# Kernel optimization log

Measured on AMD Instinct MI355X. Metric: run time of the kernel, lower is better.

Reference implementation:

```python
import jax, jax.numpy as jnp
from jax import lax
import numpy as np

B, C, H, W = 4, 64, 64, 64
D_STATE, D_CONV = 16, 4


def setup_inputs() -> dict:
    key = jax.random.key(0)
    ks = iter(jax.random.split(key, 64))
    def rnd(shape, s=0.02):
        return jax.random.normal(next(ks), shape, jnp.float32) * s
    inp = {}
    inp["x"] = jax.random.normal(next(ks), (B, C, H, W), jnp.float32)
    # LayerNorm((C,H,W)) affine params
    inp["n1_w"] = jnp.ones((C, H, W), jnp.float32); inp["n1_b"] = jnp.zeros((C, H, W), jnp.float32)
    inp["n2_w"] = jnp.ones((C, H, W), jnp.float32); inp["n2_b"] = jnp.zeros((C, H, W), jnp.float32)
    # OSSModule projections
    inp["inproj_w"] = rnd((2 * C, C)); inp["inproj_b"] = jnp.zeros((2 * C,), jnp.float32)
    inp["dw_w"] = rnd((C, 1, 3, 3), 0.1); inp["dw_b"] = jnp.zeros((C,), jnp.float32)
    inp["outproj_w"] = rnd((C, C)); inp["outproj_b"] = jnp.zeros((C,), jnp.float32)
    # Mamba params (expand=2, d_state=16, d_conv=4, dt_rank=ceil(d_model/16))
    def mamba_p(name, d_model):
        d_inner = 2 * d_model
        dt_rank = max(1, -(-d_model // 16))
        inp[name + "_in_w"] = rnd((2 * d_inner, d_model))
        inp[name + "_conv_w"] = rnd((d_inner, 1, D_CONV), 0.1)
        inp[name + "_conv_b"] = jnp.zeros((d_inner,), jnp.float32)
        inp[name + "_xproj_w"] = rnd((dt_rank + 2 * D_STATE, d_inner))
        inp[name + "_dt_w"] = rnd((d_inner, dt_rank), dt_rank ** -0.5)
        inp[name + "_dt_b"] = jnp.full((d_inner,), -4.6, jnp.float32)  # softplus -> ~0.01
        inp[name + "_Alog"] = jnp.log(jnp.tile(jnp.arange(1, D_STATE + 1, dtype=jnp.float32), (d_inner, 1)))
        inp[name + "_D"] = jnp.ones((d_inner,), jnp.float32)
        inp[name + "_out_w"] = rnd((d_model, d_inner))
    mamba_p("m1", 4 * C)
    mamba_p("m2", 2)
    # EFFN (hidden = 2*C)
    hid = 2 * C
    inp["ffn_in_w"] = rnd((2 * hid, C)); inp["ffn_in_b"] = jnp.zeros((2 * hid,), jnp.float32)
    inp["ffn_dw_w"] = rnd((2 * hid, 1, 3, 3), 0.1); inp["ffn_dw_b"] = jnp.zeros((2 * hid,), jnp.float32)
    inp["ffn_out_w"] = rnd((C, hid)); inp["ffn_out_b"] = jnp.zeros((C,), jnp.float32)
    return inp


def layernorm(x, w, b, eps=1e-5):
    mu = x.mean((1, 2, 3), keepdims=True)
    var = ((x - mu) ** 2).mean((1, 2, 3), keepdims=True)
    return (x - mu) * lax.rsqrt(var + eps) * w + b


def conv1x1(x, w, b):
    return jnp.einsum('oi,bihw->bohw', w, x) + b[None, :, None, None]


def dwconv3(x, w, b):
    y = lax.conv_general_dilated(x, w, (1, 1), [(1, 1), (1, 1)],
                                 dimension_numbers=('NCHW', 'OIHW', 'NCHW'),
                                 feature_group_count=x.shape[1])
    return y + b[None, :, None, None]


def mamba(u, in_w, conv_w, conv_b, xproj_w, dt_w, dt_b, Alog, Dp, out_w):
    # u: (B, L, d_model) -> (B, L, d_model); faithful mamba_ssm Mamba forward
    Bt, L, _ = u.shape
    d_inner = Alog.shape[0]
    dt_rank = dt_w.shape[1]
    xz = u @ in_w.T
    xi, z = jnp.split(xz, 2, axis=-1)
    # causal depthwise conv over the sequence axis
    xc = lax.conv_general_dilated(xi.transpose(0, 2, 1), conv_w, (1,), [(D_CONV - 1, 0)],
                                  dimension_numbers=('NCH', 'OIH', 'NCH'),
                                  feature_group_count=d_inner)
    xi = jax.nn.silu(xc.transpose(0, 2, 1) + conv_b)
    x_dbl = xi @ xproj_w.T
    dt = jax.nn.softplus(x_dbl[..., :dt_rank] @ dt_w.T + dt_b)      # (B,L,d_inner)
    Bm = x_dbl[..., dt_rank:dt_rank + D_STATE]                      # (B,L,d_state)
    Cm = x_dbl[..., dt_rank + D_STATE:]                             # (B,L,d_state)
    A = -jnp.exp(Alog)                                              # (d_inner,d_state)
    dA = jnp.exp(dt[..., None] * A)                                 # (B,L,d_inner,d_state)
    dBu = (dt * xi)[..., None] * Bm[:, :, None, :]                  # (B,L,d_inner,d_state)
    def step(hst, t):
        dA_t, dBu_t, C_t = t
        hst = dA_t * hst + dBu_t
        return hst, jnp.einsum('bds,bs->bd', hst, C_t)
    h0 = jnp.zeros((Bt, d_inner, D_STATE), u.dtype)
    _, ys = lax.scan(step, h0, (dA.transpose(1, 0, 2, 3), dBu.transpose(1, 0, 2, 3), Cm.transpose(1, 0, 2)))
    y = ys.transpose(1, 0, 2) + xi * Dp
    y = y * jax.nn.silu(z)
    return y @ out_w.T


def reference(x, n1_w, n1_b, n2_w, n2_b, inproj_w, inproj_b, dw_w, dw_b, outproj_w, outproj_b,
              m1_in_w, m1_conv_w, m1_conv_b, m1_xproj_w, m1_dt_w, m1_dt_b, m1_Alog, m1_D, m1_out_w,
              m2_in_w, m2_conv_w, m2_conv_b, m2_xproj_w, m2_dt_w, m2_dt_b, m2_Alog, m2_D, m2_out_w,
              ffn_in_w, ffn_in_b, ffn_dw_w, ffn_dw_b, ffn_out_w, ffn_out_b):
    b, c2, h, w = x.shape
    c = c2
    # --- OSS module branch (pre-norm) ---
    xn = layernorm(x, n1_w, n1_b)
    fo = conv1x1(xn, inproj_w, inproj_b)
    fo1, fo2 = jnp.split(fo, 2, axis=1)
    fo1 = jax.nn.silu(dwconv3(fo1, dw_w, dw_b))
    fo2 = jax.nn.silu(fo2)
    # omni selective scan: 4 directional flattenings concatenated on channels
    hf = fo1.transpose(0, 2, 3, 1).reshape(b, h * w, c)   # row-major (h_forward)
    wf = fo1.transpose(0, 3, 2, 1).reshape(b, h * w, c)   # col-major (w_forward)
    fop = jnp.concatenate([hf, hf[:, ::-1], wf, wf[:, ::-1]], axis=2)  # (b, hw, 4c)
    fop = mamba(fop, m1_in_w, m1_conv_w, m1_conv_b, m1_xproj_w, m1_dt_w, m1_dt_b, m1_Alog, m1_D, m1_out_w)
    fop = fop.reshape(b, h * w, 4, c).sum(2)
    fop = fop.transpose(0, 2, 1).reshape(b, c, h, w)
    residual = fop * fo2
    foc = residual.mean((2, 3))[:, :, None]               # adaptive_avg_pool2d -> (b,c,1)
    foc = jnp.concatenate([foc, foc[:, ::-1]], axis=2)    # (b, c, 2)
    foc = mamba(foc, m2_in_w, m2_conv_w, m2_conv_b, m2_xproj_w, m2_dt_w, m2_dt_b, m2_Alog, m2_D, m2_out_w)
    foc = foc.sum(2)[:, :, None, None]
    foss = foc * residual + residual
    x = conv1x1(foss, outproj_w, outproj_b) + x
    # --- EFFN branch (pre-norm) ---
    g = layernorm(x, n2_w, n2_b)
    g = conv1x1(g, ffn_in_w, ffn_in_b)
    g = dwconv3(g, ffn_dw_w, ffn_dw_b)
    g1, g2 = jnp.split(g, 2, axis=1)
    g = jax.nn.gelu(g1, approximate=False) * g2
    g = conv1x1(g, ffn_out_w, ffn_out_b)
    return g + x
```

## Files before the change

### kernel.cpp

```cpp
#include <hip/hip_runtime.h>
#include <math.h>


#define DEV static __device__ __forceinline__

DEV float silu_f(float x){ return x / (1.f + __expf(-x)); }

DEV ushort f2bf(float f){
  uint u = __float_as_uint(f);
  uint r = (u + 0x7FFF + ((u>>16)&1)) >> 16;
  return (ushort)r;
}
DEV uint f2bf2(float lo, float hi){
  return (uint)f2bf(lo) | ((uint)f2bf(hi)<<16);
}
DEV float bf2f(ushort u){ return __uint_as_float(((uint)u)<<16); }
DEV float bflo(uint u){ return __uint_as_float(u<<16); }
DEV float bfhi(uint u){ return __uint_as_float(u&0xffff0000u); }

typedef __attribute__((ext_vector_type(8))) short bf8_t;
typedef __attribute__((ext_vector_type(4))) float f4_t;

DEV float quad_sum4(float v){
  v += __int_as_float(__builtin_amdgcn_update_dpp(0, __float_as_int(v), 0xB1, 0xF, 0xF, false));
  v += __int_as_float(__builtin_amdgcn_update_dpp(0, __float_as_int(v), 0x4E, 0xF, 0xF, false));
  return v;
}
template<int O> DEV uint qb(uint v){
  return (uint)__builtin_amdgcn_update_dpp(0, (int)v, O*0x55, 0xF, 0xF, false);
}

__global__ __launch_bounds__(256) void ln_part(const float* __restrict__ x,
                                               float2* __restrict__ part){
  int blk = blockIdx.x; int b = blk>>6, pc = blk&63;
  const float* p = x + (size_t)b*262144 + (size_t)pc*4096;
  float s=0.f, s2=0.f;
  #pragma unroll
  for(int it=0; it<4; ++it){
    int i = threadIdx.x + it*256;
    float4 v = *(const float4*)(p + i*4);
    s  += v.x+v.y+v.z+v.w;
    s2 += v.x*v.x+v.y*v.y+v.z*v.z+v.w*v.w;
  }
  __shared__ float ls[256], ls2[256];
  ls[threadIdx.x]=s; ls2[threadIdx.x]=s2; __syncthreads();
  for(int st=128;st>0;st>>=1){
    if(threadIdx.x<st){ ls[threadIdx.x]+=ls[threadIdx.x+st]; ls2[threadIdx.x]+=ls2[threadIdx.x+st]; }
    __syncthreads();
  }
  if(threadIdx.x==0) part[blk]=make_float2(ls[0],ls2[0]);
}
__global__ __launch_bounds__(64) void ln_fin(const float2* __restrict__ part,
                                             float* __restrict__ mu, float* __restrict__ rstd){
  int b = blockIdx.x;
  float2 v = part[b*64+threadIdx.x];
  __shared__ double ds_[64], ds2_[64];
  ds_[threadIdx.x]=v.x; ds2_[threadIdx.x]=v.y; __syncthreads();
  for(int st=32;st>0;st>>=1){
    if(threadIdx.x<st){ ds_[threadIdx.x]+=ds_[threadIdx.x+st]; ds2_[threadIdx.x]+=ds2_[threadIdx.x+st]; }
    __syncthreads();
  }
  if(threadIdx.x==0){
    double m = ds_[0]*(1.0/262144.0);
    double var = ds2_[0]*(1.0/262144.0) - m*m;
    mu[b]=(float)m; rstd[b]=(float)(1.0/sqrt(var+1e-5));
  }
}

__global__ __launch_bounds__(256) void ln1_inproj(const float* __restrict__ x,
    const float* __restrict__ n1w, const float* __restrict__ n1b,
    const float* __restrict__ ipw, const float* __restrict__ ipb,
    const float* __restrict__ mu, const float* __restrict__ rstd,
    float* __restrict__ fo1_raw, float* __restrict__ fo2s){
  int bh = blockIdx.x; int b = bh>>6, h = bh&63;
  __shared__ float xn[64][64];
  __shared__ float wl[128*64];
  float m = mu[b], rs = rstd[b];
  for(int i=threadIdx.x;i<4096;i+=256){
    int c=i>>6, w=i&63;
    size_t sp=(size_t)c*4096 + h*64 + w;
    float v = x[(size_t)b*262144 + sp];
    xn[c][w] = (v-m)*rs*n1w[sp] + n1b[sp];
  }
  for(int i=threadIdx.x;i<8192;i+=256) wl[i]=ipw[i];
  __syncthreads();
  int px = threadIdx.x & 63, ob = (threadIdx.x>>6)*32;
  float acc[32];
  #pragma unroll
  for(int j=0;j<32;j++) acc[j]=0.f;
  for(int c=0;c<64;c++){
    float xv = xn[c][px];
    #pragma unroll
    for(int j=0;j<32;j++) acc[j] = fmaf(wl[(ob+j)*64+c], xv, acc[j]);
  }
  for(int j=0;j<32;j++){
    int o = ob+j;
    float v = acc[j] + ipb[o];
    if(o<64) fo1_raw[((size_t)(b*64+o))*4096 + h*64 + px] = v;
    else     fo2s  [((size_t)(b*64+o-64))*4096 + h*64 + px] = silu_f(v);
  }
}

__global__ __launch_bounds__(256) void dwconv_silu_tr(const float* __restrict__ src_,
    const float* __restrict__ dww, const float* __restrict__ dwb,
    ushort* __restrict__ fo1s, ushort* __restrict__ fo1t){
  int bc = blockIdx.x; int c = bc & 63;
  const float* src = src_ + (size_t)bc*4096;
  float wk[9];
  #pragma unroll
  for(int k=0;k<9;k++) wk[k]=dww[c*9+k];
  float bias = dwb[c];
  __shared__ float tl[64][65];
  for(int i=threadIdx.x;i<4096;i+=256){
    int h=i>>6, w=i&63;
    float acc=bias;
    #pragma unroll
    for(int kh=0;kh<3;kh++){
      int ih=h+kh-1; if(ih<0||ih>63) continue;
      #pragma unroll
      for(int kw=0;kw<3;kw++){
        int iw=w+kw-1; if(iw<0||iw>63) continue;
        acc += wk[kh*3+kw]*src[ih*64+iw];
      }
    }
    tl[h][w] = silu_f(acc);
  }
  __syncthreads();
  ushort* ps = fo1s + (size_t)bc*4096;
  ushort* pt = fo1t + (size_t)bc*4096;
  for(int i=threadIdx.x;i<4096;i+=256){
    ps[i] = f2bf(tl[i>>6][i&63]);
    pt[i] = f2bf(tl[i&63][i>>6]);
  }
}

__global__ __launch_bounds__(256) void cvt_w_bf(const float* __restrict__ w, uint* __restrict__ wb){
  int i = blockIdx.x*256 + threadIdx.x;
  float2 v = *(const float2*)(w + 2*i);
  wb[i] = f2bf2(v.x, v.y);
}
__global__ __launch_bounds__(256) void wdt_make(const float* __restrict__ dtw,
    const float* __restrict__ xpw, ushort* __restrict__ wcomb){
  int d = blockIdx.x;
  float wr[16];
  #pragma unroll
  for(int r=0;r<16;r++) wr[r]=dtw[d*16+r];
  for(int k=threadIdx.x;k<512;k+=256){
    float acc=0.f;
    #pragma unroll
    for(int r=0;r<16;r++) acc = fmaf(wr[r], xpw[r*512+k], acc);
    wcomb[(size_t)d*512+k]=f2bf(acc);
  }
}
__global__ __launch_bounds__(256) void cvt_bc_pad(const float* __restrict__ xpw, ushort* __restrict__ wcomb){
  int i = blockIdx.x*256 + threadIdx.x;
  int row = i>>9, k = i&511;
  float v = (row<32) ? xpw[8192 + row*512 + k] : 0.f;
  wcomb[(size_t)(512+row)*512 + k] = f2bf(v);
}
__global__ __launch_bounds__(256) void fold_w_bf(const float* __restrict__ ow, ushort* __restrict__ wf){
  int i = blockIdx.x*256 + threadIdx.x;
  int c = i>>9, d2 = i&511;
  wf[i] = f2bf(ow[c*512+d2] + ow[(64+c)*512+d2] + ow[(128+c)*512+d2] + ow[(192+c)*512+d2]);
}
__global__ __launch_bounds__(256) void cvt_fiw(const float* __restrict__ w, ushort* __restrict__ wb){
  int i = blockIdx.x*256 + threadIdx.x;
  wb[i] = f2bf(w[i]);
}

__global__ __launch_bounds__(256) void gather_u_t(const ushort* __restrict__ fo1s,
    const ushort* __restrict__ fo1t, uint* __restrict__ u_bf){
  int blk = blockIdx.x;
  int lt = blk&63, part = (blk>>6)&3, b = blk>>8;
  int l0 = lt<<6;
  const ushort* s = (part<2)? fo1s : fo1t;
  bool rev = part&1;
  __shared__ ushort tl[64][65];
  for(int i=threadIdx.x;i<4096;i+=256){
    int c=i>>6, j=i&63;
    int l = l0 + j;
    int idx = rev ? (4095-l) : l;
    tl[c][j] = s[((size_t)(b*64+c))*4096 + idx];
  }
  __syncthreads();
  for(int i=threadIdx.x;i<2048;i+=256){
    int j = i>>5, cp = i&31;
    int l = l0 + j;
    u_bf[((size_t)(b*4096)+l)*128 + part*32 + cp] = (uint)tl[2*cp][j] | ((uint)tl[2*cp+1][j]<<16);
  }
}

__global__ __launch_bounds__(256) void gemm_xz_mfma(const ushort* __restrict__ u_bf,
    const ushort* __restrict__ w_bf, ushort* __restrict__ xi0_bf, ushort* __restrict__ z_bf){
  int blk = blockIdx.x; int b = blk>>5; int l0 = (blk&31)<<7;
  int o0 = blockIdx.y<<7;
  __shared__ __align__(16) ushort Al[2][5120];
  __shared__ __align__(16) ushort Bl[2][5120];
  int t = threadIdx.x, lane = t&63, wid = t>>6;
  int wr = wid>>1, wc = wid&1;
  int rl = lane&15, kseg = (lane>>4)*8;
  f4_t acc[4][4];
  #pragma unroll
  for(int m=0;m<4;m++)
    #pragma unroll
    for(int n=0;n<4;n++) acc[m][n]=(f4_t){0.f,0.f,0.f,0.f};

  int r0 = t>>2, r1 = 64+(t>>2), seg = t&3;
  uint4 rA0,rA1,rB0,rB1;
  auto issue=[&](int kc){
    rA0 = *(const uint4*)&w_bf[(size_t)(o0+r0)*256 + kc*32 + seg*8];
    rA1 = *(const uint4*)&w_bf[(size_t)(o0+r1)*256 + kc*32 + seg*8];
    rB0 = *(const uint4*)&u_bf[((size_t)(b*4096)+l0+r0)*256 + kc*32 + seg*8];
    rB1 = *(const uint4*)&u_bf[((size_t)(b*4096)+l0+r1)*256 + kc*32 + seg*8];
  };
  auto store=[&](int buf){
    *(uint4*)&Al[buf][r0*40 + seg*8] = rA0;
    *(uint4*)&Al[buf][r1*40 + seg*8] = rA1;
    *(uint4*)&Bl[buf][r0*40 + seg*8] = rB0;
    *(uint4*)&Bl[buf][r1*40 + seg*8] = rB1;
  };
  issue(0); store(0); __syncthreads();
  int buf=0;
  for(int kc=0;kc<8;kc++){
    bool more = kc<7;
    if(more) issue(kc+1);
    bf8_t af[4], bfr[4];
    #pragma unroll
    for(int m=0;m<4;m++) af[m] = *(const bf8_t*)&Al[buf][(wr*64+m*16+rl)*40 + kseg];
    #pragma unroll
    for(int n=0;n<4;n++) bfr[n] = *(const bf8_t*)&Bl[buf][(wc*64+n*16+rl)*40 + kseg];
    #pragma unroll
    for(int m=0;m<4;m++)
      #pragma unroll
      for(int n=0;n<4;n++)
        acc[m][n] = __builtin_amdgcn_mfma_f32_16x16x32_bf16(af[m], bfr[n], acc[m][n], 0,0,0);
    __syncthreads();
    if(more){ store(buf^1); __syncthreads(); }
    buf^=1;
  }
  int orow = (lane>>4)*4;
  if(o0 < 512){
    #pragma unroll
    for(int m=0;m<4;m++)
      #pragma unroll
      for(int n=0;n<4;n++){
        int l = l0 + wc*64 + n*16 + rl;
        #pragma unroll
        for(int r=0;r<4;r++){
          int o = o0 + wr*64 + m*16 + orow + r;
          xi0_bf[((size_t)(b*512)+o)*4096 + l] = f2bf(acc[m][n][r]);
        }
      }
  } else {
    #pragma unroll
    for(int m=0;m<4;m++)
      #pragma unroll
      for(int n=0;n<4;n++){
        int l = l0 + wc*64 + n*16 + rl;
        int gz = (o0 - 512 + wr*64 + m*16) >> 4;
        uint2 pkz;
        pkz.x = f2bf2(acc[m][n][0], acc[m][n][1]);
        pkz.y = f2bf2(acc[m][n][2], acc[m][n][3]);
        *(uint2*)&z_bf[(((size_t)(b*32)+gz)*4096 + l)*16 + orow] = pkz;
      }
  }
}

__global__ __launch_bounds__(256) void conv1d_silu2(const ushort* __restrict__ xi0,
    const float* __restrict__ cw, const float* __restrict__ cb,
    ushort* __restrict__ xi_c, ushort* __restrict__ xi_l){
  int blk = blockIdx.x;
  int lt = blk&63, dt8 = (blk>>6)&7, b = blk>>9;
  int d0 = dt8*64, l0 = lt*64;
  __shared__ float T[64][65];
  int t = threadIdx.x, lloc = t&63, dq = t>>6;
// ... 168 lines not shown
    step2(qb<3>(pkc[0]),qb<3>(pkc[1]),24);
    step2(qb<3>(pkc[2]),qb<3>(pkc[3]),26);
    step2(qb<3>(pkc[4]),qb<3>(pkc[5]),28);
    step2(qb<3>(pkc[6]),qb<3>(pkc[7]),30);
    if(t<1){ pack(); storeB(); }
  }
  int idx = blk*64 + lane;
  Pbuf[idx]=make_float4(exp2f(A2[0]*S), exp2f(A2[1]*S), exp2f(A2[2]*S), exp2f(A2[3]*S));
  qbuf[idx]=make_float4(q[0],q[1],q[2],q[3]);
}

__global__ __launch_bounds__(256) void scan3_mid(const float4* __restrict__ Pbuf,
    const float4* __restrict__ qbuf, float4* __restrict__ hstart){
  int tid = blockIdx.x*256+threadIdx.x;
  int lane = tid&63, sg = tid>>6;
  float4 h = make_float4(0.f,0.f,0.f,0.f);
  #pragma unroll 8
  for(int c=0;c<64;c++){
    int idx = (sg*64+c)*64 + lane;
    hstart[idx]=h;
    float4 P=Pbuf[idx], q=qbuf[idx];
    h.x = fmaf(P.x,h.x,q.x);
    h.y = fmaf(P.y,h.y,q.y);
    h.z = fmaf(P.z,h.z,q.z);
    h.w = fmaf(P.w,h.w,q.w);
  }
}

__global__ __launch_bounds__(64) void scan3_p2(
    const ushort* __restrict__ dtx, const ushort* __restrict__ xix,
    const ushort* __restrict__ z_bf, const ushort* __restrict__ bc,
    const float* __restrict__ Alog, const float* __restrict__ Dp,
    const float4* __restrict__ hstart, ushort* __restrict__ y_bf){
  int blk=blockIdx.x;
  int c=blk&63, g=(blk>>6)&31, b=blk>>11;
  int lane=threadIdx.x, ch=lane>>2, sq=lane&3;
  int d=g*16+ch;
  float4 Ar = *(const float4*)(Alog + d*16 + sq*4);
  float A2[4];
  A2[0]=-__expf(Ar.x)*1.44269504088896f;
  A2[1]=-__expf(Ar.y)*1.44269504088896f;
  A2[2]=-__expf(Ar.z)*1.44269504088896f;
  A2[3]=-__expf(Ar.w)*1.44269504088896f;
  float Dv = Dp[d];
  int je = lane>>1, halfe = lane&1;
  __shared__ __align__(16) float bcl[32][36];
  __shared__ __align__(16) float pl[32][18];
  const int l0c = c*64;
  const size_t dtrow = ((size_t)(b*512)+d)*4096;
  const ushort* xb = bc + (size_t)b*4096*32;
  const size_t zybase = (((size_t)(b*32)+g)*4096);
  uint4 rdt, rxi; uint2 rbc[4];
  uint4 rzb[2];
  uint pkc[8];
  auto issue=[&](int t){
    int l0 = l0c + t*32;
    rdt = *(const uint4*)(dtx + dtrow + l0 + sq*8);
    rxi = *(const uint4*)(xix + dtrow + l0 + sq*8);
    #pragma unroll
    for(int k=0;k<4;k++){
      int j=(lane>>3)+k*8, seg=lane&7;
      rbc[k]=*(const uint2*)(xb + (size_t)(l0+j)*32 + seg*4);
    }
    rzb[t&1] = *(const uint4*)&z_bf[(zybase + l0 + je)*16 + halfe*8];
  };
  auto pack=[&](){
    const uint* dp=(const uint*)&rdt; const uint* xp=(const uint*)&rxi;
    #pragma unroll
    for(int k=0;k<4;k++){
      uint ud=dp[k], ux=xp[k];
      pkc[2*k]   = (ud&0xffffu)|(ux<<16);
      pkc[2*k+1] = (ud>>16)|(ux&0xffff0000u);
    }
  };
  auto storeBC=[&](){
    #pragma unroll
    for(int k=0;k<4;k++){
      float4 v = make_float4(bflo(rbc[k].x), bfhi(rbc[k].x), bflo(rbc[k].y), bfhi(rbc[k].y));
      *(float4*)&bcl[(lane>>3)+k*8][(lane&7)*4] = v;
    }
  };
  float h[4];
  {
    float4 h0 = hstart[blk*64 + lane];
    h[0]=h0.x; h[1]=h0.y; h[2]=h0.z; h[3]=h0.w;
  }
  auto step2=[&](uint p0, uint p1, int j0){
    {
      float4 B4 = *(const float4*)&bcl[j0][sq*4];
      float4 C4 = *(const float4*)&bcl[j0][16+sq*4];
      float dtv=bflo(p0), xiv=bfhi(p0); float u=dtv*xiv;
      float p;
      #pragma unroll
      for(int i=0;i<4;i++){ float dA=exp2f(dtv*A2[i]); h[i]=fmaf(dA,h[i],u*((const float*)&B4)[i]); }
      p = h[0]*C4.x; p=fmaf(h[1],C4.y,p); p=fmaf(h[2],C4.z,p); p=fmaf(h[3],C4.w,p);
      p = quad_sum4(p);
      if(sq==0) pl[j0][ch] = p + xiv*Dv;
    }
    {
      float4 B4 = *(const float4*)&bcl[j0+1][sq*4];
      float4 C4 = *(const float4*)&bcl[j0+1][16+sq*4];
      float dtv=bflo(p1), xiv=bfhi(p1); float u=dtv*xiv;
      float p;
      #pragma unroll
      for(int i=0;i<4;i++){ float dA=exp2f(dtv*A2[i]); h[i]=fmaf(dA,h[i],u*((const float*)&B4)[i]); }
      p = h[0]*C4.x; p=fmaf(h[1],C4.y,p); p=fmaf(h[2],C4.z,p); p=fmaf(h[3],C4.w,p);
      p = quad_sum4(p);
      if(sq==0) pl[j0+1][ch] = p + xiv*Dv;
    }
  };
  issue(0); pack(); storeBC();
  for(int t=0;t<2;t++){
    if(t<1) issue(t+1);
    step2(qb<0>(pkc[0]),qb<0>(pkc[1]), 0);
    step2(qb<0>(pkc[2]),qb<0>(pkc[3]), 2);
    step2(qb<0>(pkc[4]),qb<0>(pkc[5]), 4);
    step2(qb<0>(pkc[6]),qb<0>(pkc[7]), 6);
    step2(qb<1>(pkc[0]),qb<1>(pkc[1]), 8);
    step2(qb<1>(pkc[2]),qb<1>(pkc[3]),10);
    step2(qb<1>(pkc[4]),qb<1>(pkc[5]),12);
    step2(qb<1>(pkc[6]),qb<1>(pkc[7]),14);
    step2(qb<2>(pkc[0]),qb<2>(pkc[1]),16);
    step2(qb<2>(pkc[2]),qb<2>(pkc[3]),18);
    step2(qb<2>(pkc[4]),qb<2>(pkc[5]),20);
    step2(qb<2>(pkc[6]),qb<2>(pkc[7]),22);
    step2(qb<3>(pkc[0]),qb<3>(pkc[1]),24);
    step2(qb<3>(pkc[2]),qb<3>(pkc[3]),26);
    step2(qb<3>(pkc[4]),qb<3>(pkc[5]),28);
    step2(qb<3>(pkc[6]),qb<3>(pkc[7]),30);
    {
      int l = l0c + t*32 + je;
      uint4 zr = rzb[t&1];
      const ushort* zp = (const ushort*)&zr;
      float pv[8];
      #pragma unroll
      for(int k=0;k<4;k++){
        float2 v2 = *(const float2*)&pl[je][halfe*8+2*k];
        pv[2*k]=v2.x; pv[2*k+1]=v2.y;
      }
      float yv[8];
      #pragma unroll
      for(int k=0;k<8;k++) yv[k] = pv[k] * silu_f(bf2f(zp[k]));
      uint4 yo;
      uint* yp=(uint*)&yo;
      yp[0]=f2bf2(yv[0],yv[1]); yp[1]=f2bf2(yv[2],yv[3]);
      yp[2]=f2bf2(yv[4],yv[5]); yp[3]=f2bf2(yv[6],yv[7]);
      *(uint4*)&y_bf[((size_t)zybase + l)*16 + halfe*8] = yo;
    }
    if(t<1){ pack(); storeBC(); }
  }
}

__global__ __launch_bounds__(256) void gemm_res_mfma(const ushort* __restrict__ y_bf,
    const ushort* __restrict__ wf_bf, const float* __restrict__ fo2s, ushort* __restrict__ res_l){
  int blk = blockIdx.x; int b = blk>>5; int l0 = (blk&31)<<7;
  __shared__ __align__(16) ushort Wl[2][2560];
  __shared__ __align__(16) ushort Yl[2][5120];
  int t = threadIdx.x, lane = t&63, wid = t>>6;
  int rl = lane&15, kseg = (lane>>4)*8;
  f4_t acc[4][2];
  #pragma unroll
  for(int m=0;m<4;m++)
    #pragma unroll
    for(int n=0;n<2;n++) acc[m][n]=(f4_t){0.f,0.f,0.f,0.f};
  int ry = t>>1;
  int rw = t>>2, sgw = t&3;
  uint4 rY0, rY1, rW;
  auto issue=[&](int kc){
    int gg = 2*kc + (t&1);
    const ushort* yrow = &y_bf[(((size_t)(b*32)+gg)*4096 + l0+ry)*16];
    rY0 = *(const uint4*)&yrow[0];
    rY1 = *(const uint4*)&yrow[8];
    rW  = *(const uint4*)&wf_bf[(size_t)rw*512 + kc*32 + sgw*8];
  };
  auto store=[&](int buf){
    *(uint4*)&Yl[buf][ry*40 + (t&1)*16]     = rY0;
    *(uint4*)&Yl[buf][ry*40 + (t&1)*16 + 8] = rY1;
    *(uint4*)&Wl[buf][rw*40 + sgw*8]        = rW;
  };
  issue(0); store(0); __syncthreads();
  int buf=0;
  for(int kc=0;kc<16;kc++){
    bool more = kc<15;
    if(more) issue(kc+1);
    bf8_t aw[4], by[2];
    #pragma unroll
    for(int m=0;m<4;m++) aw[m] = *(const bf8_t*)&Wl[buf][(m*16+rl)*40 + kseg];
    #pragma unroll
    for(int n=0;n<2;n++) by[n] = *(const bf8_t*)&Yl[buf][(wid*32+n*16+rl)*40 + kseg];
    #pragma unroll
    for(int m=0;m<4;m++)
      #pragma unroll
      for(int n=0;n<2;n++)
        acc[m][n] = __builtin_amdgcn_mfma_f32_16x16x32_bf16(aw[m], by[n], acc[m][n], 0,0,0);
    __syncthreads();
    if(more){ store(buf^1); __syncthreads(); }
    buf^=1;
  }
  int orow = (lane>>4)*4;
  #pragma unroll
  for(int m=0;m<4;m++)
    #pragma unroll
    for(int n=0;n<2;n++){
      int l = l0 + wid*32 + n*16 + rl;
      float vals[4];
      #pragma unroll
      for(int r=0;r<4;r++){
        int o = m*16 + orow + r;
        size_t idx = ((size_t)(b*64+o))*4096 + l;
        vals[r] = acc[m][n][r]*fo2s[idx];
      }
      uint2 pk2;
      pk2.x = f2bf2(vals[0], vals[1]);
      pk2.y = f2bf2(vals[2], vals[3]);
      *(uint2*)&res_l[((size_t)(b*4096)+l)*64 + m*16 + orow] = pk2;
    }
}

__global__ __launch_bounds__(256) void colmean_l(const ushort* __restrict__ res_l,
    float* __restrict__ cpart){
  int blk=blockIdx.x;
  int ck=blk&15, b=blk>>4;
  int t=threadIdx.x, c=t&63, q=t>>6;
  const ushort* base = res_l + ((size_t)(b*4096) + ck*256)*64;
  float s=0.f;
  for(int i=0;i<64;i++) s += bf2f(base[(size_t)(q + 4*i)*64 + c]);
  __shared__ float ls[4][64];
  ls[q][c]=s; __syncthreads();
  if(t<64) cpart[(size_t)blk*64 + t] = ls[0][t]+ls[1][t]+ls[2][t]+ls[3][t];
}
__global__ __launch_bounds__(256) void colmean_fin(const float* __restrict__ cpart,
    float* __restrict__ fm){
  int t=threadIdx.x; int b=t>>6, c=t&63;
  float s=0.f;
  for(int ck=0;ck<16;ck++) s += cpart[(size_t)(b*16+ck)*64 + c];
  fm[t] = s*(1.f/4096.f);
}

__global__ __launch_bounds__(64) void mamba2_kernel(const float* __restrict__ fm,
    const float* __restrict__ in_w, const float* __restrict__ cw, const float* __restrict__ cb,
    const float* __restrict__ xp, const float* __restrict__ dtw, const float* __restrict__ dtb,
    const float* __restrict__ Alog, const float* __restrict__ Dp, const float* __restrict__ ow,
    float* __restrict__ fsum){
  int b = blockIdx.x; int t = threadIdx.x;
  __shared__ float xi0m[64][4], xim[64][4], dtm[64][4], xbl[64][33], ym[64][4];
  float a0 = fm[b*64+t], a1 = fm[b*64 + 63-t];
  float zreg[4];
  #pragma unroll
  for(int d2=0;d2<4;d2++){
    xi0m[t][d2] = in_w[d2*2+0]*a0 + in_w[d2*2+1]*a1;
    zreg[d2]    = in_w[(4+d2)*2+0]*a0 + in_w[(4+d2)*2+1]*a1;
  }
  __syncthreads();
  float xir[4];
  #pragma unroll
  for(int d2=0;d2<4;d2++){
    float acc=cb[d2];
    #pragma unroll
    for(int k=0;k<4;k++){
      int srow=t-3+k;
      if(srow>=0) acc += cw[d2*4+k]*xi0m[srow][d2];
    }
    xir[d2]=silu_f(acc);
    xim[t][d2]=xir[d2];
  }
  for(int j=0;j<33;j++){
    float acc=0;
    #pragma unroll
    for(int d2=0;d2<4;d2++) acc += xp[j*4+d2]*xir[d2];
    xbl[t][j]=acc;
  }
  #pragma unroll
  for(int d2=0;d2<4;d2++){
    float v = xbl[t][0]*dtw[d2] + dtb[d2];
    dtm[t][d2] = (v>20.f)? v : log1pf(__expf(v));
  }
  __syncthreads();
  int dd=t>>4, s=t&15;
  float A2 = -__expf(Alog[dd*16+s]) * 1.44269504088896f;
  float h=0.f;
  for(int c=0;c<64;c++){
    float dtv=dtm[c][dd];
    float dA=exp2f(dtv*A2);
    h = fmaf(dA, h, dtv*xim[c][dd]*xbl[c][1+s]);
    float p = h*xbl[c][17+s];
    p += __shfl_xor(p,1,16);
    p += __shfl_xor(p,2,16);
    p += __shfl_xor(p,4,16);
    p += __shfl_xor(p,8,16);
    if(s==0) ym[c][dd]=p;
  }
  __syncthreads();
  float os=0.f;
  #pragma unroll
  for(int d2=0;d2<4;d2++){
    float yv = (ym[t][d2] + xim[t][d2]*Dp[d2]) * silu_f(zreg[d2]);
    os += yv * (ow[d2] + ow[4+d2]);
  }
  fsum[b*64+t]=os;
}

__global__ __launch_bounds__(256) void outproj_mfma(const ushort* __restrict__ res_l,
    const float* __restrict__ fsum, const ushort* __restrict__ opw_bf, const float* __restrict__ opb,
    const float* __restrict__ x, float* __restrict__ x2, float2* __restrict__ part){
  int blk = blockIdx.x; int b = blk>>6; int lt = blk&63; int l0 = lt<<6;
  __shared__ __align__(16) ushort Al[2][2560];
  __shared__ __align__(16) ushort Bl[2][2560];
  __shared__ float sf[64];
  __shared__ float ls[256], ls2[256];
  int t = threadIdx.x, lane = t&63, wid = t>>6;
  int wo = wid>>1, wl = wid&1;
  int rl = lane&15, kseg = (lane>>4)*8;
  if(t<64) sf[t] = 1.f + fsum[b*64+t];
  __syncthreads();
  f4_t acc[2][2];
  #pragma unroll
  for(int m=0;m<2;m++)
    #pragma unroll
    for(int n=0;n<2;n++) acc[m][n]=(f4_t){0.f,0.f,0.f,0.f};
  int r = t>>2, seg = t&3;
  uint4 rA,rB; int rkc=0;
  auto issue=[&](int kc){
    rkc = kc;
    rA = *(const uint4*)&opw_bf[(size_t)r*64 + kc*32 + seg*8];
    rB = *(const uint4*)&res_l[((size_t)(b*4096)+l0+r)*64 + kc*32 + seg*8];
  };
  auto store=[&](int buf){
    *(uint4*)&Al[buf][r*40 + seg*8] = rA;
    const ushort* pb = (const ushort*)&rB;
    uint4 ob;
    uint* op = (uint*)&ob;
    #pragma unroll
    for(int j=0;j<4;j++){
      int kb = rkc*32 + seg*8 + 2*j;
      float lo = bf2f(pb[2*j])   * sf[kb];
      float hi = bf2f(pb[2*j+1]) * sf[kb+1];
      op[j] = f2bf2(lo, hi);
    }
    *(uint4*)&Bl[buf][r*40 + seg*8] = ob;
  };
  issue(0); store(0); __syncthreads();
  int buf=0;
  for(int kc=0;kc<2;kc++){
    bool more = kc<1;
    if(more) issue(kc+1);
    bf8_t af[2], bfr[2];
    #pragma unroll
    for(int m=0;m<2;m++) af[m] = *(const bf8_t*)&Al[buf][(wo*32+m*16+rl)*40 + kseg];
    #pragma unroll
    for(int n=0;n<2;n++) bfr[n] = *(const bf8_t*)&Bl[buf][(wl*32+n*16+rl)*40 + kseg];
    #pragma unroll
    for(int m=0;m<2;m++)
      #pragma unroll
      for(int n=0;n<2;n++)
        acc[m][n] = __builtin_amdgcn_mfma_f32_16x16x32_bf16(af[m], bfr[n], acc[m][n], 0,0,0);
    __syncthreads();
    if(more){ store(buf^1); __syncthreads(); }
    buf^=1;
  }
  int orow = (lane>>4)*4;
  float s=0.f, s2=0.f;
  #pragma unroll
  for(int m=0;m<2;m++)
    #pragma unroll
    for(int n=0;n<2;n++){
      int l = l0 + wl*32 + n*16 + rl;
      #pragma unroll
      for(int rr=0;rr<4;rr++){
        int og = wo*32 + m*16 + orow + rr;
        size_t idx = ((size_t)(b*64+og))*4096 + l;
        float v = acc[m][n][rr] + opb[og] + x[idx];
        x2[idx]=v;
        s += v; s2 = fmaf(v,v,s2);
      }
    }
  ls[t]=s; ls2[t]=s2; __syncthreads();
  for(int st=128;st>0;st>>=1){
    if(t<st){ ls[t]+=ls[t+st]; ls2[t]+=ls2[t+st]; }
    __syncthreads();
  }
  if(t==0) part[b*64+lt]=make_float2(ls[0],ls2[0]);
}

__global__ __launch_bounds__(256) void ln2_apply_bf(const float* __restrict__ x2,
    const float* __restrict__ n2w, const float* __restrict__ n2b,
    const float* __restrict__ mu2, const float* __restrict__ rstd2,
    uint* __restrict__ xn_bf){
  int bh=blockIdx.x; int b=bh>>6,h=bh&63;
  __shared__ float tl[64][65];
  float m=mu2[b], rs=rstd2[b];
  for(int i=threadIdx.x;i<4096;i+=256){
    int c=i>>6,w=i&63;
    size_t sp=(size_t)c*4096 + h*64 + w;
    tl[c][w]=(x2[(size_t)b*262144+sp]-m)*rs*n2w[sp]+n2b[sp];
  }
  __syncthreads();
  for(int i=threadIdx.x;i<2048;i+=256){
    int w=i>>5, cp=i&31;
    xn_bf[((size_t)(b*4096)+h*64+w)*32 + cp] = f2bf2(tl[2*cp][w], tl[2*cp+1][w]);
  }
}

__global__ __launch_bounds__(256) void gemm_ffn_mfma(const ushort* __restrict__ xn_bf,
    const ushort* __restrict__ fiw_bf, const float* __restrict__ fib,
    ushort* __restrict__ g_bf){
  int blk = blockIdx.x; int b = blk>>6; int l0 = (blk&63)<<6;
  int o0 = blockIdx.y<<6;
  __shared__ __align__(16) ushort Al[2][2560];
  __shared__ __align__(16) ushort Bl[2][2560];
  int t = threadIdx.x, lane = t&63, wid = t>>6;
  int wo = wid>>1, wl = wid&1;
  int rl = lane&15, kseg = (lane>>4)*8;
  f4_t acc[2][2];
  #pragma unroll
  for(int m=0;m<2;m++)
    #pragma unroll
    for(int n=0;n<2;n++) acc[m][n]=(f4_t){0.f,0.f,0.f,0.f};
  int r = t>>2, seg = t&3;
  uint4 rA,rB;
  auto issue=[&](int kc){
    rA = *(const uint4*)&fiw_bf[(size_t)(o0+r)*64 + kc*32 + seg*8];
    rB = *(const uint4*)&xn_bf[((size_t)(b*4096)+l0+r)*64 + kc*32 + seg*8];
  };
  auto store=[&](int buf){
    *(uint4*)&Al[buf][r*40 + seg*8] = rA;
    *(uint4*)&Bl[buf][r*40 + seg*8] = rB;
  };
  issue(0); store(0); __syncthreads();
  int buf=0;
  for(int kc=0;kc<2;kc++){
    bool more = kc<1;
    if(more) issue(kc+1);
    bf8_t af[2], bfr[2];
    #pragma unroll
    for(int m=0;m<2;m++) af[m] = *(const bf8_t*)&Al[buf][(wo*32+m*16+rl)*40 + kseg];
    #pragma unroll
    for(int n=0;n<2;n++) bfr[n] = *(const bf8_t*)&Bl[buf][(wl*32+n*16+rl)*40 + kseg];
    #pragma unroll
    for(int m=0;m<2;m++)
      #pragma unroll
      for(int n=0;n<2;n++)
        acc[m][n] = __builtin_amdgcn_mfma_f32_16x16x32_bf16(af[m], bfr[n], acc[m][n], 0,0,0);
    __syncthreads();
    if(more){ store(buf^1); __syncthreads(); }
    buf^=1;
  }
  int orow = (lane>>4)*4;
  #pragma unroll
  for(int m=0;m<2;m++)
    #pragma unroll
    for(int n=0;n<2;n++){
      int l = l0 + wl*32 + n*16 + rl;
      #pragma unroll
      for(int rr=0;rr<4;rr++){
        int og = o0 + wo*32 + m*16 + orow + rr;
        g_bf[((size_t)(b*256+og))*4096 + l] = f2bf(acc[m][n][rr] + fib[og]);
      }
    }
}

__global__ __launch_bounds__(256) void ffn_dw_gate(const ushort* __restrict__ g,
    const float* __restrict__ dww, const float* __restrict__ dwb, ushort* __restrict__ gm){
  int blk = blockIdx.x;
  int j = blk & 127, b = blk >> 7;
  __shared__ float P0[66][66];
  __shared__ float P1[66][66];
  int t = threadIdx.x;
  for(int i=t;i<4356;i+=256){ ((float*)P0)[i]=0.f; ((float*)P1)[i]=0.f; }
  __syncthreads();
  const ushort* g0 = g + ((size_t)(b*256+j))*4096;
  const ushort* g1 = g + ((size_t)(b*256+j+128))*4096;
  for(int i=t;i<4096;i+=256){
    int h=i>>6, w=i&63;
    P0[h+1][w+1] = bf2f(g0[i]);
    P1[h+1][w+1] = bf2f(g1[i]);
  }
  __syncthreads();
  float wk0[9], wk1[9];
  #pragma unroll
  for(int k=0;k<9;k++){ wk0[k]=dww[j*9+k]; wk1[k]=dww[(j+128)*9+k]; }
  float b0=dwb[j], b1=dwb[j+128];
  int w = t&63, hq = t>>6;
  int wp = w+1, h0 = hq*16;
  float a0[3][3], a1[3][3];
  #pragma unroll
  for(int r=0;r<2;r++)
    #pragma unroll
    for(int c=0;c<3;c++){ a0[r][c]=P0[h0+r][wp-1+c]; a1[r][c]=P1[h0+r][wp-1+c]; }
  ushort* gout = gm + ((size_t)(b*128+j))*4096;
  for(int i=0;i<16;i++){
    int h=h0+i;
    #pragma unroll
    for(int c=0;c<3;c++){ a0[2][c]=P0[h+2][wp-1+c]; a1[2][c]=P1[h+2][wp-1+c]; }
    float acc0=b0, acc1=b1;
    #pragma unroll
    for(int r=0;r<3;r++)
      #pragma unroll
      for(int c=0;c<3;c++){
        acc0=fmaf(wk0[r*3+c],a0[r][c],acc0);
        acc1=fmaf(wk1[r*3+c],a1[r][c],acc1);
      }
    float ge = 0.5f*acc0*(1.f+erff(acc0*0.70710678f));
    gout[h*64+w] = f2bf(ge*acc1);
    #pragma unroll
    for(int c=0;c<3;c++){
      a0[0][c]=a0[1][c]; a0[1][c]=a0[2][c];
      a1[0][c]=a1[1][c]; a1[1][c]=a1[2][c];
    }
  }
}

__global__ __launch_bounds__(256) void ffn_out_kernel(const ushort* __restrict__ gm,
    const float* __restrict__ fow, const float* __restrict__ fob,
    const float* __restrict__ x2, float* __restrict__ out){
  int bh=blockIdx.x; int b=bh>>6,h=bh&63;
  __shared__ float tile[128][64];
  __shared__ float wl[64*128];
  for(int i=threadIdx.x;i<8192;i+=256){
    int c=i>>6,w=i&63;
    tile[c][w]=bf2f(gm[((size_t)(b*128+c))*4096 + h*64 + w]);
  }
  for(int i=threadIdx.x;i<8192;i+=256) wl[i]=fow[i];
  __syncthreads();
  int px=threadIdx.x&63, og=threadIdx.x>>6;
  float acc[16];
  #pragma unroll
  for(int j=0;j<16;j++) acc[j]=0.f;
  for(int c=0;c<128;c++){
    float v=tile[c][px];
    #pragma unroll
    for(int j=0;j<16;j++) acc[j]=fmaf(wl[(og*16+j)*128+c],v,acc[j]);
  }
  for(int j=0;j<16;j++){
    int o=og*16+j;
    size_t idx=((size_t)(b*64+o))*4096 + h*64 + px;
    out[idx]=acc[j]+fob[o]+x2[idx];
  }
}

extern "C" void kernel_launch(void* const* d_in, const int* in_sizes, int n_in,
                              void* d_out, int out_size, void* d_ws, size_t ws_size,
                              hipStream_t stream){
  const float* x      = (const float*)d_in[0];
  const float* n1w    = (const float*)d_in[1];
  const float* n1b    = (const float*)d_in[2];
  const float* n2w    = (const float*)d_in[3];
  const float* n2b    = (const float*)d_in[4];
  const float* ipw    = (const float*)d_in[5];
  const float* ipb    = (const float*)d_in[6];
  const float* dww    = (const float*)d_in[7];
  const float* dwb    = (const float*)d_in[8];
  const float* opw    = (const float*)d_in[9];
  const float* opb    = (const float*)d_in[10];
  const float* m1_inw = (const float*)d_in[11];
  const float* m1_cw  = (const float*)d_in[12];
  const float* m1_cb  = (const float*)d_in[13];
  const float* m1_xp  = (const float*)d_in[14];
  const float* m1_dtw = (const float*)d_in[15];
  const float* m1_dtb = (const float*)d_in[16];
  const float* m1_Al  = (const float*)d_in[17];
  const float* m1_D   = (const float*)d_in[18];
  const float* m1_ow  = (const float*)d_in[19];
  const float* m2_inw = (const float*)d_in[20];
  const float* m2_cw  = (const float*)d_in[21];
  const float* m2_cb  = (const float*)d_in[22];
  const float* m2_xp  = (const float*)d_in[23];
  const float* m2_dtw = (const float*)d_in[24];
  const float* m2_dtb = (const float*)d_in[25];
  const float* m2_Al  = (const float*)d_in[26];
  const float* m2_D   = (const float*)d_in[27];
  const float* m2_ow  = (const float*)d_in[28];
  const float* fiw    = (const float*)d_in[29];
  const float* fib    = (const float*)d_in[30];
  const float* fdw    = (const float*)d_in[31];
  const float* fdb    = (const float*)d_in[32];
  const float* fow    = (const float*)d_in[33];
  const float* fob    = (const float*)d_in[34];
  float* out = (float*)d_out;
  float* ws  = (float*)d_ws;

  const size_t M1 = 1048576;
  float* mu1   = ws + 0;  float* rstd1 = ws + 4;
  float* mu2   = ws + 8;  float* rstd2 = ws + 12;
  float* fmean = ws + 64;
  float* fsum  = ws + 320;
  float* cpart = ws + 1024;
  float* lnpart= ws + 33792;
  float* base0 = ws + 36864;
  float* fo1raw= base0;
  float* fo2s  = base0 + M1;
  float* fo1s  = base0 + 2*M1;
  float* fo1t  = base0 + 3*M1;
  float* big0  = base0 + 4*M1;
  float* big1  = base0 + 12*M1;
  float* big2  = base0 + 20*M1;
  float* big3  = base0 + 28*M1;
  float* bcslot= base0 + 36*M1;
  float* x2    = base0 + 36*M1 + 524288;
  float* tail  = x2 + M1;
  ushort* w_bf    = (ushort*)tail;
  ushort* wcomb   = (ushort*)(tail + 131072);
  ushort* wf_bf   = (ushort*)(tail + 278528);
  ushort* fiw_bf  = (ushort*)(tail + 294912);
  ushort* opw_bf  = (ushort*)(tail + 303104);

  uint*   u_bf  = (uint*)big0;
  ushort* dt_bf = (ushort*)big0;
  ushort* g_bf  = (ushort*)big0;
  float*  hstart= big0 + 4*M1;
  ushort* xi0_bf= (ushort*)big1;
  ushort* y_bf  = (ushort*)big1;
  ushort* gm_bf = (ushort*)(big1 + 4*M1);
  ushort* z_bf  = (ushort*)big2;
  ushort* xi_l  = (ushort*)(big2 + 4*M1);
  ushort* xi_c  = (ushort*)big3;
  float*  Pbuf  = big3 + 4*M1;
  float*  qbuf  = big3 + 6*M1;
  ushort* bc_bf = (ushort*)bcslot;
  uint*   xn2_bf= (uint*)fo1s;
  ushort* fo1s_bf = (ushort*)fo1s;
  ushort* fo1t_bf = (ushort*)fo1t;
  ushort* res_l = (ushort*)fo1raw;

  hipLaunchKernelGGL(ln_part, dim3(256), dim3(256), 0, stream, x, (float2*)lnpart);
  hipLaunchKernelGGL(ln_fin, dim3(4), dim3(64), 0, stream, (const float2*)lnpart, mu1, rstd1);
  hipLaunchKernelGGL(cvt_w_bf, dim3(512), dim3(256), 0, stream, m1_inw, (uint*)w_bf);
  hipLaunchKernelGGL(wdt_make, dim3(512), dim3(256), 0, stream, m1_dtw, m1_xp, wcomb);
  hipLaunchKernelGGL(cvt_bc_pad, dim3(128), dim3(256), 0, stream, m1_xp, wcomb);
  hipLaunchKernelGGL(fold_w_bf, dim3(128), dim3(256), 0, stream, m1_ow, wf_bf);
  hipLaunchKernelGGL(cvt_fiw, dim3(64), dim3(256), 0, stream, fiw, fiw_bf);
  hipLaunchKernelGGL(cvt_fiw, dim3(16), dim3(256), 0, stream, opw, opw_bf);
  hipLaunchKernelGGL(ln1_inproj, dim3(256), dim3(256), 0, stream,
                     x, n1w, n1b, ipw, ipb, mu1, rstd1, fo1raw, fo2s);
  hipLaunchKernelGGL(dwconv_silu_tr, dim3(256), dim3(256), 0, stream,
                     fo1raw, dww, dwb, fo1s_bf, fo1t_bf);
  hipLaunchKernelGGL(gather_u_t, dim3(1024), dim3(256), 0, stream, fo1s_bf, fo1t_bf, u_bf);
  hipLaunchKernelGGL(gemm_xz_mfma, dim3(128, 8), dim3(256), 0, stream,
                     (const ushort*)u_bf, w_bf, xi0_bf, z_bf);
  hipLaunchKernelGGL(conv1d_silu2, dim3(2048), dim3(256), 0, stream,
                     xi0_bf, m1_cw, m1_cb, xi_c, xi_l);
  hipLaunchKernelGGL(gemm_proj_mfma, dim3(256, 9), dim3(256), 0, stream,
                     xi_l, wcomb, m1_dtb, dt_bf, bc_bf);
  hipLaunchKernelGGL(scan3_p1, dim3(8192), dim3(64), 0, stream,
                     dt_bf, xi_c, bc_bf, m1_Al, (float4*)Pbuf, (float4*)qbuf);
  hipLaunchKernelGGL(scan3_mid, dim3(32), dim3(256), 0, stream,
                     (const float4*)Pbuf, (const float4*)qbuf, (float4*)hstart);
  hipLaunchKernelGGL(scan3_p2, dim3(8192), dim3(64), 0, stream,
                     dt_bf, xi_c, z_bf, bc_bf, m1_Al, m1_D, (const float4*)hstart, y_bf);
  hipLaunchKernelGGL(gemm_res_mfma, dim3(128), dim3(256), 0, stream,
                     y_bf, wf_bf, fo2s, res_l);
  hipLaunchKernelGGL(colmean_l, dim3(64), dim3(256), 0, stream, res_l, cpart);
  hipLaunchKernelGGL(colmean_fin, dim3(1), dim3(256), 0, stream, cpart, fmean);
  hipLaunchKernelGGL(mamba2_kernel, dim3(4), dim3(64), 0, stream,
                     fmean, m2_inw, m2_cw, m2_cb, m2_xp, m2_dtw, m2_dtb, m2_Al, m2_D, m2_ow, fsum);
  hipLaunchKernelGGL(outproj_mfma, dim3(256), dim3(256), 0, stream,
                     res_l, fsum, opw_bf, opb, x, x2, (float2*)lnpart);
  hipLaunchKernelGGL(ln_fin, dim3(4), dim3(64), 0, stream, (const float2*)lnpart, mu2, rstd2);
  hipLaunchKernelGGL(ln2_apply_bf, dim3(256), dim3(256), 0, stream,
                     x2, n2w, n2b, mu2, rstd2, xn2_bf);
  hipLaunchKernelGGL(gemm_ffn_mfma, dim3(256, 4), dim3(256), 0, stream,
                     (const ushort*)xn2_bf, fiw_bf, fib, g_bf);
  hipLaunchKernelGGL(ffn_dw_gate, dim3(512), dim3(256), 0, stream, g_bf, fdw, fdb, gm_bf);
  hipLaunchKernelGGL(ffn_out_kernel, dim3(256), dim3(256), 0, stream, gm_bf, fow, fob, x2, out);
}
```

Baseline: 347.3 us.

## Split LN1+in-proj into bf16 LN apply and MFMA GEMM with bf16 outputs

The fused scalar-FMA LayerNorm plus 128x64 input projection kernel is replaced by a generic LN-apply kernel that writes channel-last bf16 activations, followed by an MFMA bf16 GEMM. The in-proj weight is converted to bf16 up front, and the fo1/fo2 intermediates are now stored as bf16 instead of fp32, which halves their traffic for the depthwise conv and residual GEMM. This adds an extra launch and an intermediate round trip through memory, and lowers the precision of the projection outputs.

```diff
diff --git a/kernel.cpp b/kernel.cpp
--- a/kernel.cpp
+++ b/kernel.cpp
@@ -67,45 +67,90 @@
   }
 }
 
-__global__ __launch_bounds__(256) void ln1_inproj(const float* __restrict__ x,
-    const float* __restrict__ n1w, const float* __restrict__ n1b,
-    const float* __restrict__ ipw, const float* __restrict__ ipb,
+__global__ __launch_bounds__(256) void ln_apply_bf(const float* __restrict__ xin,
+    const float* __restrict__ nw, const float* __restrict__ nb,
     const float* __restrict__ mu, const float* __restrict__ rstd,
-    float* __restrict__ fo1_raw, float* __restrict__ fo2s){
-  int bh = blockIdx.x; int b = bh>>6, h = bh&63;
-  __shared__ float xn[64][64];
-  __shared__ float wl[128*64];
-  float m = mu[b], rs = rstd[b];
+    uint* __restrict__ xn_bf){
+  int bh=blockIdx.x; int b=bh>>6,h=bh&63;
+  __shared__ float tl[64][65];
+  float m=mu[b], rs=rstd[b];
   for(int i=threadIdx.x;i<4096;i+=256){
-    int c=i>>6, w=i&63;
+    int c=i>>6,w=i&63;
     size_t sp=(size_t)c*4096 + h*64 + w;
-    float v = x[(size_t)b*262144 + sp];
-    xn[c][w] = (v-m)*rs*n1w[sp] + n1b[sp];
-  }
-  for(int i=threadIdx.x;i<8192;i+=256) wl[i]=ipw[i];
+    tl[c][w]=(xin[(size_t)b*262144+sp]-m)*rs*nw[sp]+nb[sp];
+  }
   __syncthreads();
-  int px = threadIdx.x & 63, ob = (threadIdx.x>>6)*32;
-  float acc[32];
-  #pragma unroll
-  for(int j=0;j<32;j++) acc[j]=0.f;
-  for(int c=0;c<64;c++){
-    float xv = xn[c][px];
-    #pragma unroll
-    for(int j=0;j<32;j++) acc[j] = fmaf(wl[(ob+j)*64+c], xv, acc[j]);
-  }
-  for(int j=0;j<32;j++){
-    int o = ob+j;
-    float v = acc[j] + ipb[o];
-    if(o<64) fo1_raw[((size_t)(b*64+o))*4096 + h*64 + px] = v;
-    else     fo2s  [((size_t)(b*64+o-64))*4096 + h*64 + px] = silu_f(v);
-  }
-}
-
-__global__ __launch_bounds__(256) void dwconv_silu_tr(const float* __restrict__ src_,
+  for(int i=threadIdx.x;i<2048;i+=256){
+    int w=i>>5, cp=i&31;
+    xn_bf[((size_t)(b*4096)+h*64+w)*32 + cp] = f2bf2(tl[2*cp][w], tl[2*cp+1][w]);
+  }
+}
+
+__global__ __launch_bounds__(256) void gemm_in_mfma(const ushort* __restrict__ xn_bf,
+    const ushort* __restrict__ ipw_bf, const float* __restrict__ ipb,
+    ushort* __restrict__ fo1p, ushort* __restrict__ fo2s){
+  int blk = blockIdx.x; int b = blk>>6; int l0 = (blk&63)<<6;
+  int o0 = blockIdx.y<<6;
+  __shared__ __align__(16) ushort Al[2][2560];
+  __shared__ __align__(16) ushort Bl[2][2560];
+  int t = threadIdx.x, lane = t&63, wid = t>>6;
+  int wo = wid>>1, wl = wid&1;
+  int rl = lane&15, kseg = (lane>>4)*8;
+  f4_t acc[2][2];
+  #pragma unroll
+  for(int m=0;m<2;m++)
+    #pragma unroll
+    for(int n=0;n<2;n++) acc[m][n]=(f4_t){0.f,0.f,0.f,0.f};
+  int r = t>>2, seg = t&3;
+  uint4 rA,rB;
+  auto issue=[&](int kc){
+    rA = *(const uint4*)&ipw_bf[(size_t)(o0+r)*64 + kc*32 + seg*8];
+    rB = *(const uint4*)&xn_bf[((size_t)(b*4096)+l0+r)*64 + kc*32 + seg*8];
+  };
+  auto store=[&](int buf){
+    *(uint4*)&Al[buf][r*40 + seg*8] = rA;
+    *(uint4*)&Bl[buf][r*40 + seg*8] = rB;
+  };
+  issue(0); store(0); __syncthreads();
+  int buf=0;
+  for(int kc=0;kc<2;kc++){
+    bool more = kc<1;
+    if(more) issue(kc+1);
+    bf8_t af[2], bfr[2];
+    #pragma unroll
+    for(int m=0;m<2;m++) af[m] = *(const bf8_t*)&Al[buf][(wo*32+m*16+rl)*40 + kseg];
+    #pragma unroll
+    for(int n=0;n<2;n++) bfr[n] = *(const bf8_t*)&Bl[buf][(wl*32+n*16+rl)*40 + kseg];
+    #pragma unroll
+    for(int m=0;m<2;m++)
+      #pragma unroll
+      for(int n=0;n<2;n++)
+        acc[m][n] = __builtin_amdgcn_mfma_f32_16x16x32_bf16(af[m], bfr[n], acc[m][n], 0,0,0);
+    __syncthreads();
+    if(more){ store(buf^1); __syncthreads(); }
+    buf^=1;
+  }
+  int orow = (lane>>4)*4;
+  #pragma unroll
+  for(int m=0;m<2;m++)
+    #pragma unroll
+    for(int n=0;n<2;n++){
+      int l = l0 + wl*32 + n*16 + rl;
+      #pragma unroll
+      for(int rr=0;rr<4;rr++){
+        int og = o0 + wo*32 + m*16 + orow + rr;
+        float v = acc[m][n][rr] + ipb[og];
+        if(og<64) fo1p[((size_t)(b*64+og))*4096 + l] = f2bf(v);
+        else      fo2s[((size_t)(b*64+og-64))*4096 + l] = f2bf(silu_f(v));
+      }
+    }
+}
+
+__global__ __launch_bounds__(256) void dwconv_silu_tr(const ushort* __restrict__ src_,
     const float* __restrict__ dww, const float* __restrict__ dwb,
     ushort* __restrict__ fo1s, ushort* __restrict__ fo1t){
   int bc = blockIdx.x; int c = bc & 63;
-  const float* src = src_ + (size_t)bc*4096;
+  const ushort* src = src_ + (size_t)bc*4096;
   float wk[9];
   #pragma unroll
   for(int k=0;k<9;k++) wk[k]=dww[c*9+k];
@@ -120,7 +165,7 @@
       #pragma unroll
       for(int kw=0;kw<3;kw++){
         int iw=w+kw-1; if(iw<0||iw>63) continue;
-        acc += wk[kh*3+kw]*src[ih*64+iw];
+        acc += wk[kh*3+kw]*bf2f(src[ih*64+iw]);
       }
     }
     tl[h][w] = silu_f(acc);
@@ -595,7 +640,7 @@
 }
 
 __global__ __launch_bounds__(256) void gemm_res_mfma(const ushort* __restrict__ y_bf,
-    const ushort* __restrict__ wf_bf, const float* __restrict__ fo2s, ushort* __restrict__ res_l){
+    const ushort* __restrict__ wf_bf, const ushort* __restrict__ fo2s, ushort* __restrict__ res_l){
   int blk = blockIdx.x; int b = blk>>5; int l0 = (blk&31)<<7;
   __shared__ __align__(16) ushort Wl[2][2560];
   __shared__ __align__(16) ushort Yl[2][5120];
@@ -651,7 +696,7 @@
       for(int r=0;r<4;r++){
         int o = m*16 + orow + r;
         size_t idx = ((size_t)(b*64+o))*4096 + l;
-        vals[r] = acc[m][n][r]*fo2s[idx];
+        vals[r] = acc[m][n][r]*bf2f(fo2s[idx]);
       }
       uint2 pk2;
       pk2.x = f2bf2(vals[0], vals[1]);
@@ -823,25 +868,6 @@
     __syncthreads();
   }
   if(t==0) part[b*64+lt]=make_float2(ls[0],ls2[0]);
-}
-
-__global__ __launch_bounds__(256) void ln2_apply_bf(const float* __restrict__ x2,
-    const float* __restrict__ n2w, const float* __restrict__ n2b,
-    const float* __restrict__ mu2, const float* __restrict__ rstd2,
-    uint* __restrict__ xn_bf){
-  int bh=blockIdx.x; int b=bh>>6,h=bh&63;
-  __shared__ float tl[64][65];
-  float m=mu2[b], rs=rstd2[b];
-  for(int i=threadIdx.x;i<4096;i+=256){
-    int c=i>>6,w=i&63;
-    size_t sp=(size_t)c*4096 + h*64 + w;
-    tl[c][w]=(x2[(size_t)b*262144+sp]-m)*rs*n2w[sp]+n2b[sp];
-  }
-  __syncthreads();
-  for(int i=threadIdx.x;i<2048;i+=256){
-    int w=i>>5, cp=i&31;
-    xn_bf[((size_t)(b*4096)+h*64+w)*32 + cp] = f2bf2(tl[2*cp][w], tl[2*cp+1][w]);
-  }
 }
 
 __global__ __launch_bounds__(256) void gemm_ffn_mfma(const ushort* __restrict__ xn_bf,
@@ -1046,11 +1072,13 @@
   ushort* wf_bf   = (ushort*)(tail + 278528);
   ushort* fiw_bf  = (ushort*)(tail + 294912);
   ushort* opw_bf  = (ushort*)(tail + 303104);
+  ushort* ipw_bf  = (ushort*)(tail + 305152);
 
   uint*   u_bf  = (uint*)big0;
   ushort* dt_bf = (ushort*)big0;
   ushort* g_bf  = (ushort*)big0;
   float*  hstart= big0 + 4*M1;
+  uint*   xn1_bf= (uint*)big1;
   ushort* xi0_bf= (ushort*)big1;
   ushort* y_bf  = (ushort*)big1;
   ushort* gm_bf = (ushort*)(big1 + 4*M1);
@@ -1061,6 +1089,8 @@
   float*  qbuf  = big3 + 6*M1;
   ushort* bc_bf = (ushort*)bcslot;
   uint*   xn2_bf= (uint*)fo1s;
+  ushort* fo1p_bf = (ushort*)fo1raw;
+  ushort* fo2s_bf = (ushort*)fo2s;
   ushort* fo1s_bf = (ushort*)fo1s;
   ushort* fo1t_bf = (ushort*)fo1t;
   ushort* res_l = (ushort*)fo1raw;
@@ -1073,10 +1103,13 @@
   hipLaunchKernelGGL(fold_w_bf, dim3(128), dim3(256), 0, stream, m1_ow, wf_bf);
   hipLaunchKernelGGL(cvt_fiw, dim3(64), dim3(256), 0, stream, fiw, fiw_bf);
   hipLaunchKernelGGL(cvt_fiw, dim3(16), dim3(256), 0, stream, opw, opw_bf);
-  hipLaunchKernelGGL(ln1_inproj, dim3(256), dim3(256), 0, stream,
-                     x, n1w, n1b, ipw, ipb, mu1, rstd1, fo1raw, fo2s);
+  hipLaunchKernelGGL(cvt_fiw, dim3(32), dim3(256), 0, stream, ipw, ipw_bf);
+  hipLaunchKernelGGL(ln_apply_bf, dim3(256), dim3(256), 0, stream,
+                     x, n1w, n1b, mu1, rstd1, xn1_bf);
+  hipLaunchKernelGGL(gemm_in_mfma, dim3(256, 2), dim3(256), 0, stream,
+                     (const ushort*)xn1_bf, ipw_bf, ipb, fo1p_bf, fo2s_bf);
   hipLaunchKernelGGL(dwconv_silu_tr, dim3(256), dim3(256), 0, stream,
-                     fo1raw, dww, dwb, fo1s_bf, fo1t_bf);
+                     fo1p_bf, dww, dwb, fo1s_bf, fo1t_bf);
   hipLaunchKernelGGL(gather_u_t, dim3(1024), dim3(256), 0, stream, fo1s_bf, fo1t_bf, u_bf);
   hipLaunchKernelGGL(gemm_xz_mfma, dim3(128, 8), dim3(256), 0, stream,
                      (const ushort*)u_bf, w_bf, xi0_bf, z_bf);
@@ -1091,7 +1124,7 @@
   hipLaunchKernelGGL(scan3_p2, dim3(8192), dim3(64), 0, stream,
                      dt_bf, xi_c, z_bf, bc_bf, m1_Al, m1_D, (const float4*)hstart, y_bf);
   hipLaunchKernelGGL(gemm_res_mfma, dim3(128), dim3(256), 0, stream,
-                     y_bf, wf_bf, fo2s, res_l);
+                     y_bf, wf_bf, fo2s_bf, res_l);
   hipLaunchKernelGGL(colmean_l, dim3(64), dim3(256), 0, stream, res_l, cpart);
   hipLaunchKernelGGL(colmean_fin, dim3(1), dim3(256), 0, stream, cpart, fmean);
   hipLaunchKernelGGL(mamba2_kernel, dim3(4), dim3(64), 0, stream,
@@ -1099,7 +1132,7 @@
   hipLaunchKernelGGL(outproj_mfma, dim3(256), dim3(256), 0, stream,
                      res_l, fsum, opw_bf, opb, x, x2, (float2*)lnpart);
   hipLaunchKernelGGL(ln_fin, dim3(4), dim3(64), 0, stream, (const float2*)lnpart, mu2, rstd2);
-  hipLaunchKernelGGL(ln2_apply_bf, dim3(256), dim3(256), 0, stream,
+  hipLaunchKernelGGL(ln_apply_bf, dim3(256), dim3(256), 0, stream,
                      x2, n2w, n2b, mu2, rstd2, xn2_bf);
   hipLaunchKernelGGL(gemm_ffn_mfma, dim3(256, 4), dim3(256), 0, stream,
                      (const ushort*)xn2_bf, fiw_bf, fib, g_bf);
```

After: 340.9 us. About the same (-1.8%).
